# Kernel tuning notes

Measured on AMD Instinct MI355X. Metric: run time of the kernel, lower is better.

## Reference

```python
import jax, jax.numpy as jnp
import numpy as np

NUM_EMBEDDINGS = 512
EMBEDDING_DIM = 64
COMMITMENT_COST = 0.25


def setup_inputs() -> dict:
    key = jax.random.key(0)
    k1, k2, k3 = jax.random.split(key, 3)
    inputs = jax.random.normal(k1, (32, 64, 64, 64), dtype=jnp.float32)  # NCHW, C=embedding_dim
    labels = jax.random.randint(k2, (32,), 0, 12, dtype=jnp.int64 if jax.config.jax_enable_x64 else jnp.int32)
    # embedding initialized uniform(-1/K, 1/K) as in the torch module
    embedding = jax.random.uniform(k3, (NUM_EMBEDDINGS, EMBEDDING_DIM), dtype=jnp.float32,
                                   minval=-1.0 / NUM_EMBEDDINGS, maxval=1.0 / NUM_EMBEDDINGS)
    return {"inputs": inputs, "labels": labels, "embedding": embedding}


def reference(inputs, labels, embedding):
    # inputs: [B, C, H, W] with C == EMBEDDING_DIM; labels unused (matches original forward)
    x = jnp.transpose(inputs, (0, 2, 3, 1))            # [B, H, W, C]
    input_shape = x.shape
    flat = x.reshape(-1, EMBEDDING_DIM)                # [N, D]

    distances = (jnp.sum(flat * flat, axis=1, keepdims=True)
                 + jnp.sum(embedding * embedding, axis=1)
                 - 2.0 * jnp.matmul(flat, embedding.T))
    encoding_indices = jnp.argmin(distances, axis=1)   # [N]
    encodings = jax.nn.one_hot(encoding_indices, NUM_EMBEDDINGS, dtype=inputs.dtype)  # [N, K]

    # gather is the same math as encodings @ embedding, without the dense matmul
    quantized = embedding[encoding_indices].reshape(input_shape)  # [B, H, W, C]

    e_latent_loss = jnp.mean((jax.lax.stop_gradient(quantized) - x) ** 2)
    q_latent_loss = jnp.mean((quantized - jax.lax.stop_gradient(x)) ** 2)
    loss = q_latent_loss + COMMITMENT_COST * e_latent_loss

    # straight-through estimator
    quantized_st = x + jax.lax.stop_gradient(quantized - x)

    avg_probs = jnp.mean(encodings, axis=0)
    perplexity = jnp.exp(-jnp.sum(avg_probs * jnp.log(avg_probs + 1e-10)))

    return (loss, jnp.transpose(quantized_st, (0, 3, 1, 2)), perplexity, encodings)
```

## Files before the change

### kernel.cpp

```cpp
#include <hip/hip_runtime.h>


#define OFF_Q    1
#define OFF_PERP 8388609
#define OFF_ENC  8388610

typedef float accf4 __attribute__((ext_vector_type(4)));
typedef short bfrag8 __attribute__((ext_vector_type(8)));

__device__ __forceinline__ unsigned short f2bf(float f) {
    union { float f; unsigned u; } v; v.f = f;
    unsigned r = v.u + 0x7FFFu + ((v.u >> 16) & 1u);
    return (unsigned short)(r >> 16);
}

__device__ __forceinline__ void lds_barrier() {
    asm volatile("s_waitcnt lgkmcnt(0)" ::: "memory");
    __builtin_amdgcn_s_barrier();
    asm volatile("" ::: "memory");
}

__global__ __launch_bounds__(512) void vq_prep(const float* __restrict__ emb,
                                               float* __restrict__ Bk,
                                               unsigned* __restrict__ counts) {
    int k = threadIdx.x;
    const float4* e4 = reinterpret_cast<const float4*>(emb) + k * 16;
    float s = 0.f;
    #pragma unroll
    for (int i = 0; i < 16; ++i) {
        float4 v = e4[i];
        s += v.x * v.x + v.y * v.y + v.z * v.z + v.w * v.w;
    }
    Bk[k] = s;
    counts[k] = 0u;
}

__global__ __launch_bounds__(512, 4) void vq_dist(const float* __restrict__ in,
                                                  const float* __restrict__ emb,
                                                  const float* __restrict__ Bk,
                                                  int* __restrict__ idx,
                                                  float* __restrict__ lossPart,
                                                  float* __restrict__ out) {
    __shared__ __align__(16) unsigned short xB[64 * 72];
    __shared__ float sdw[8][64];
    __shared__ int   skw[8][64];
    __shared__ float lossW[8];

    const int tid  = (int)threadIdx.x;
    const int lane = tid & 63;
    const int v    = __builtin_amdgcn_readfirstlane(tid >> 6);
    const int q    = lane >> 4;
    const int cidx = lane & 15;

    bfrag8 efr[4][2];
    #pragma unroll
    for (int tn = 0; tn < 4; ++tn) {
        #pragma unroll
        for (int ks = 0; ks < 2; ++ks) {
            const float* ep = emb + (size_t)(v * 64 + tn * 16 + cidx) * 64 + ks * 32 + q * 8;
            float4 e0 = *reinterpret_cast<const float4*>(ep);
            float4 e1 = *reinterpret_cast<const float4*>(ep + 4);
            bfrag8 b;
            b[0] = (short)f2bf(e0.x); b[1] = (short)f2bf(e0.y);
            b[2] = (short)f2bf(e0.z); b[3] = (short)f2bf(e0.w);
            b[4] = (short)f2bf(e1.x); b[5] = (short)f2bf(e1.y);
            b[6] = (short)f2bf(e1.z); b[7] = (short)f2bf(e1.w);
            efr[tn][ks] = b;
        }
    }
    float4 Bn[4];
    #pragma unroll
    for (int tn = 0; tn < 4; ++tn)
        Bn[tn] = *reinterpret_cast<const float4*>(&Bk[v * 64 + tn * 16 + q * 4]);
    const int kbaseLane = v * 64 + q * 4;

    float lacc = 0.f;

    #pragma unroll 1
    for (int g = 0; g < 4; ++g) {
        const int gab = (int)blockIdx.x * 4 + g;
        const int bb  = gab >> 6;
        const int hh  = gab & 63;
        const size_t rowBase = (size_t)bb * 262144 + (size_t)hh * 64 + (size_t)lane;

        bfrag8 xpk;
        #pragma unroll
        for (int cc = 0; cc < 8; ++cc) {
            const float val = in[rowBase + (size_t)(v * 8 + cc) * 4096];
            lacc += val * val;
            xpk[cc] = (short)f2bf(val);
        }
        *reinterpret_cast<bfrag8*>(&xB[lane * 72 + v * 8]) = xpk;
        lds_barrier();

        #pragma unroll
        for (int rt = 0; rt < 4; ++rt) {
            const bfrag8 x0 = *reinterpret_cast<const bfrag8*>(&xB[(rt * 16 + cidx) * 72 + q * 8]);
            const bfrag8 x1 = *reinterpret_cast<const bfrag8*>(&xB[(rt * 16 + cidx) * 72 + 32 + q * 8]);
            accf4 acc[4];
            #pragma unroll
            for (int tn = 0; tn < 4; ++tn) {
                acc[tn] = (accf4){0.f, 0.f, 0.f, 0.f};
                acc[tn] = __builtin_amdgcn_mfma_f32_16x16x32_bf16(efr[tn][0], x0, acc[tn], 0, 0, 0);
                acc[tn] = __builtin_amdgcn_mfma_f32_16x16x32_bf16(efr[tn][1], x1, acc[tn], 0, 0, 0);
            }
            float best = 3.4e38f; int bk = kbaseLane;
            #pragma unroll
            for (int tn = 0; tn < 4; ++tn) {
                #pragma unroll
                for (int r = 0; r < 4; ++r) {
                    const float Bj = (r == 0) ? Bn[tn].x : (r == 1) ? Bn[tn].y : (r == 2) ? Bn[tn].z : Bn[tn].w;
                    const float d = Bj - 2.0f * acc[tn][r];
                    if (d < best) { best = d; bk = kbaseLane + tn * 16 + r; }
                }
            }
            #pragma unroll
            for (int s = 16; s <= 32; s <<= 1) {
                const float od = __shfl_xor(best, s);
                const int   ok = __shfl_xor(bk, s);
                if (od < best || (od == best && ok < bk)) { best = od; bk = ok; }
            }
            if (q == 0) {
                sdw[v][rt * 16 + cidx] = best;
                skw[v][rt * 16 + cidx] = bk;
            }
        }
        lds_barrier();

        if (v == 0) {
            float fd = sdw[0][lane];
            int   fk = skw[0][lane];
            #pragma unroll
            for (int vv = 1; vv < 8; ++vv) {
                const float dv = sdw[vv][lane];
                const int   kv = skw[vv][lane];
                if (dv < fd) { fd = dv; fk = kv; }
            }
            idx[gab * 64 + lane] = fk;
            lacc += fd;
        }
    }

    #pragma unroll
    for (int off = 32; off > 0; off >>= 1) lacc += __shfl_down(lacc, off);
    if (lane == 0) lossW[v] = lacc;
    lds_barrier();
    if (tid == 0) {
        float s = 0.f;
        #pragma unroll
        for (int i = 0; i < 8; ++i) s += lossW[i];
        lossPart[blockIdx.x] = s;
    }
}

__global__ __launch_bounds__(256) void vq_enc(const int* __restrict__ idx,
                                              const float* __restrict__ emb,
                                              unsigned* __restrict__ counts,
                                              float* __restrict__ out) {
    __shared__ int ki[64];
    __shared__ float eqL[64 * 68];

    const int tid = (int)threadIdx.x;
    const int gab = (int)blockIdx.x;
    const int bb  = gab >> 6;
    const int hh  = gab & 63;

    if (tid < 64) ki[tid] = idx[gab * 64 + tid];
    __syncthreads();
    if (tid < 64) atomicAdd(&counts[ki[tid]], 1u);

    {
        const int row = tid >> 2, seg = tid & 3;
        const float4* ep = reinterpret_cast<const float4*>(emb + (size_t)ki[row] * 64 + seg * 16);
        float4* dst = reinterpret_cast<float4*>(&eqL[row * 68 + seg * 16]);
        #pragma unroll
        for (int i = 0; i < 4; ++i) dst[i] = ep[i];
    }
    __syncthreads();

    {
        const int w = tid & 63, cq = tid >> 6;
        const size_t qBase = OFF_Q + (size_t)bb * 262144 + (size_t)hh * 64 + (size_t)w;
        #pragma unroll
        for (int cc = 0; cc < 16; ++cc) {
            const int c = cq * 16 + cc;
            out[qBase + (size_t)c * 4096] = eqL[w * 68 + c];
        }
    }

    const int rh = tid >> 7;
    const int j2 = tid & 127;
    float2* enc2 = reinterpret_cast<float2*>(out + OFF_ENC + (size_t)gab * 32768);

    #pragma unroll 4
    for (int r2 = 0; r2 < 32; ++r2) {
        const int row = r2 * 2 + rh;
        const int k = ki[row];
        #pragma unroll
        for (int half = 0; half < 2; ++half) {
            const int jj = j2 + half * 128;
            float2 val;
            val.x = ((k >> 1) == jj && (k & 1) == 0) ? 1.0f : 0.0f;
            val.y = ((k >> 1) == jj && (k & 1) == 1) ? 1.0f : 0.0f;
            enc2[(size_t)row * 256 + jj] = val;
        }
    }
}

__global__ __launch_bounds__(512) void vq_fin(const unsigned* __restrict__ counts,
                                              const float* __restrict__ lossPart,
                                              float* __restrict__ out) {
    __shared__ float red[512];
    __shared__ float lr[512];
    int k = threadIdx.x;
    float p = (float)counts[k] * (1.0f / 131072.0f);
    red[k] = p * logf(p + 1e-10f);
    lr[k] = lossPart[k];
    __syncthreads();
    for (int s = 256; s > 0; s >>= 1) {
        if (k < s) { red[k] += red[k + s]; lr[k] += lr[k + s]; }
        __syncthreads();
    }
    if (k == 0) {
        out[OFF_PERP] = expf(-red[0]);
        float mf = lr[0] * (1.0f / 8388608.0f);
        out[0] = mf + 0.25f * mf;
    }
}

extern "C" void kernel_launch(void* const* d_in, const int* in_sizes, int n_in,
                              void* d_out, int out_size, void* d_ws, size_t ws_size,
                              hipStream_t stream) {
    const float* in  = (const float*)d_in[0];
    const float* emb = (const float*)d_in[2];
    float* out = (float*)d_out;

    float* Bk        = (float*)d_ws;
    unsigned* counts = (unsigned*)((char*)d_ws + 2048);
    float* lossPart  = (float*)((char*)d_ws + 4096);
    int* idx         = (int*)((char*)d_ws + 8192);

    vq_prep<<<1, 512, 0, stream>>>(emb, Bk, counts);
    vq_dist<<<512, 512, 0, stream>>>(in, emb, Bk, idx, lossPart, out);
    vq_enc<<<2048, 256, 0, stream>>>(idx, emb, counts, out);
    vq_fin<<<1, 512, 0, stream>>>(counts, lossPart, out);
}
```

Measured before the change: 119.7 us.

## Restructure VQ distance kernel: per-wave row tiles, stream pre-converted bf16 codebook

The distance kernel switches from splitting the codebook across 8 waves with register-resident embedding fragments to having each wave own 32 input rows and loop over all 512 codes. The codebook is converted to bf16 once in the prep kernel and streamed from global/L2. This removes the LDS staging of inputs, two block barriers and the cross-wave argmin reduction per group. In exchange, each wave re-reads the whole bf16 codebook, and the grid doubles to 1024 blocks of 256 threads, so the loss partials are summed over 1024 entries.

```diff
diff --git a/kernel.cpp b/kernel.cpp
--- a/kernel.cpp
+++ b/kernel.cpp
@@ -22,133 +22,106 @@
 
 __global__ __launch_bounds__(512) void vq_prep(const float* __restrict__ emb,
                                                float* __restrict__ Bk,
-                                               unsigned* __restrict__ counts) {
+                                               unsigned* __restrict__ counts,
+                                               unsigned* __restrict__ embB) {
     int k = threadIdx.x;
     const float4* e4 = reinterpret_cast<const float4*>(emb) + k * 16;
+    uint2* dst = reinterpret_cast<uint2*>(embB) + k * 16;
     float s = 0.f;
     #pragma unroll
     for (int i = 0; i < 16; ++i) {
         float4 v = e4[i];
         s += v.x * v.x + v.y * v.y + v.z * v.z + v.w * v.w;
+        uint2 p;
+        p.x = (unsigned)f2bf(v.x) | ((unsigned)f2bf(v.y) << 16);
+        p.y = (unsigned)f2bf(v.z) | ((unsigned)f2bf(v.w) << 16);
+        dst[i] = p;
     }
     Bk[k] = s;
     counts[k] = 0u;
 }
 
-__global__ __launch_bounds__(512, 4) void vq_dist(const float* __restrict__ in,
-                                                  const float* __restrict__ emb,
+__global__ __launch_bounds__(256, 4) void vq_dist(const float* __restrict__ in,
+                                                  const unsigned short* __restrict__ embB,
                                                   const float* __restrict__ Bk,
                                                   int* __restrict__ idx,
-                                                  float* __restrict__ lossPart,
-                                                  float* __restrict__ out) {
-    __shared__ __align__(16) unsigned short xB[64 * 72];
-    __shared__ float sdw[8][64];
-    __shared__ int   skw[8][64];
-    __shared__ float lossW[8];
+                                                  float* __restrict__ lossPart) {
+    __shared__ float lossW[4];
 
     const int tid  = (int)threadIdx.x;
     const int lane = tid & 63;
-    const int v    = __builtin_amdgcn_readfirstlane(tid >> 6);
+    const int wv   = tid >> 6;
     const int q    = lane >> 4;
     const int cidx = lane & 15;
 
-    bfrag8 efr[4][2];
-    #pragma unroll
-    for (int tn = 0; tn < 4; ++tn) {
+    const int t  = (int)blockIdx.x * 4 + wv;
+    const int bb = t >> 7;
+    const int hh = (t >> 1) & 63;
+    const int wh = t & 1;
+    const size_t base = (size_t)bb * 262144 + (size_t)hh * 64 + (size_t)wh * 32;
+
+    float lacc = 0.f;
+    bfrag8 xf[2][2];
+    #pragma unroll
+    for (int rt = 0; rt < 2; ++rt) {
         #pragma unroll
         for (int ks = 0; ks < 2; ++ks) {
-            const float* ep = emb + (size_t)(v * 64 + tn * 16 + cidx) * 64 + ks * 32 + q * 8;
-            float4 e0 = *reinterpret_cast<const float4*>(ep);
-            float4 e1 = *reinterpret_cast<const float4*>(ep + 4);
-            bfrag8 b;
-            b[0] = (short)f2bf(e0.x); b[1] = (short)f2bf(e0.y);
-            b[2] = (short)f2bf(e0.z); b[3] = (short)f2bf(e0.w);
-            b[4] = (short)f2bf(e1.x); b[5] = (short)f2bf(e1.y);
-            b[6] = (short)f2bf(e1.z); b[7] = (short)f2bf(e1.w);
-            efr[tn][ks] = b;
-        }
-    }
-    float4 Bn[4];
-    #pragma unroll
-    for (int tn = 0; tn < 4; ++tn)
-        Bn[tn] = *reinterpret_cast<const float4*>(&Bk[v * 64 + tn * 16 + q * 4]);
-    const int kbaseLane = v * 64 + q * 4;
-
-    float lacc = 0.f;
-
-    #pragma unroll 1
-    for (int g = 0; g < 4; ++g) {
-        const int gab = (int)blockIdx.x * 4 + g;
-        const int bb  = gab >> 6;
-        const int hh  = gab & 63;
-        const size_t rowBase = (size_t)bb * 262144 + (size_t)hh * 64 + (size_t)lane;
-
-        bfrag8 xpk;
-        #pragma unroll
-        for (int cc = 0; cc < 8; ++cc) {
-            const float val = in[rowBase + (size_t)(v * 8 + cc) * 4096];
-            lacc += val * val;
-            xpk[cc] = (short)f2bf(val);
-        }
-        *reinterpret_cast<bfrag8*>(&xB[lane * 72 + v * 8]) = xpk;
-        lds_barrier();
-
-        #pragma unroll
-        for (int rt = 0; rt < 4; ++rt) {
-            const bfrag8 x0 = *reinterpret_cast<const bfrag8*>(&xB[(rt * 16 + cidx) * 72 + q * 8]);
-            const bfrag8 x1 = *reinterpret_cast<const bfrag8*>(&xB[(rt * 16 + cidx) * 72 + 32 + q * 8]);
-            accf4 acc[4];
             #pragma unroll
-            for (int tn = 0; tn < 4; ++tn) {
-                acc[tn] = (accf4){0.f, 0.f, 0.f, 0.f};
-                acc[tn] = __builtin_amdgcn_mfma_f32_16x16x32_bf16(efr[tn][0], x0, acc[tn], 0, 0, 0);
-                acc[tn] = __builtin_amdgcn_mfma_f32_16x16x32_bf16(efr[tn][1], x1, acc[tn], 0, 0, 0);
+            for (int i = 0; i < 8; ++i) {
+                const float val = in[base + (size_t)(ks * 32 + q * 8 + i) * 4096 + rt * 16 + cidx];
+                lacc += val * val;
+                xf[rt][ks][i] = (short)f2bf(val);
             }
-            float best = 3.4e38f; int bk = kbaseLane;
-            #pragma unroll
-            for (int tn = 0; tn < 4; ++tn) {
-                #pragma unroll
-                for (int r = 0; r < 4; ++r) {
-                    const float Bj = (r == 0) ? Bn[tn].x : (r == 1) ? Bn[tn].y : (r == 2) ? Bn[tn].z : Bn[tn].w;
-                    const float d = Bj - 2.0f * acc[tn][r];
-                    if (d < best) { best = d; bk = kbaseLane + tn * 16 + r; }
-                }
-            }
-            #pragma unroll
-            for (int s = 16; s <= 32; s <<= 1) {
-                const float od = __shfl_xor(best, s);
-                const int   ok = __shfl_xor(bk, s);
-                if (od < best || (od == best && ok < bk)) { best = od; bk = ok; }
-            }
-            if (q == 0) {
-                sdw[v][rt * 16 + cidx] = best;
-                skw[v][rt * 16 + cidx] = bk;
-            }
-        }
-        lds_barrier();
-
-        if (v == 0) {
-            float fd = sdw[0][lane];
-            int   fk = skw[0][lane];
-            #pragma unroll
-            for (int vv = 1; vv < 8; ++vv) {
-                const float dv = sdw[vv][lane];
-                const int   kv = skw[vv][lane];
-                if (dv < fd) { fd = dv; fk = kv; }
-            }
-            idx[gab * 64 + lane] = fk;
-            lacc += fd;
-        }
+        }
+    }
+
+    float best0 = 3.4e38f, best1 = 3.4e38f;
+    int   bk0 = q * 4,     bk1 = q * 4;
+
+    #pragma unroll 4
+    for (int tile = 0; tile < 32; ++tile) {
+        const bfrag8 e0 = *reinterpret_cast<const bfrag8*>(&embB[(tile * 16 + cidx) * 64 + q * 8]);
+        const bfrag8 e1 = *reinterpret_cast<const bfrag8*>(&embB[(tile * 16 + cidx) * 64 + 32 + q * 8]);
+        accf4 a0 = (accf4){0.f, 0.f, 0.f, 0.f};
+        accf4 a1 = (accf4){0.f, 0.f, 0.f, 0.f};
+        a0 = __builtin_amdgcn_mfma_f32_16x16x32_bf16(e0, xf[0][0], a0, 0, 0, 0);
+        a0 = __builtin_amdgcn_mfma_f32_16x16x32_bf16(e1, xf[0][1], a0, 0, 0, 0);
+        a1 = __builtin_amdgcn_mfma_f32_16x16x32_bf16(e0, xf[1][0], a1, 0, 0, 0);
+        a1 = __builtin_amdgcn_mfma_f32_16x16x32_bf16(e1, xf[1][1], a1, 0, 0, 0);
+
+        const float4 B4 = *reinterpret_cast<const float4*>(&Bk[tile * 16 + q * 4]);
+        #pragma unroll
+        for (int r = 0; r < 4; ++r) {
+            const float Bj = (r == 0) ? B4.x : (r == 1) ? B4.y : (r == 2) ? B4.z : B4.w;
+            const int k = tile * 16 + q * 4 + r;
+            const float d0 = Bj - 2.0f * a0[r];
+            if (d0 < best0) { best0 = d0; bk0 = k; }
+            const float d1 = Bj - 2.0f * a1[r];
+            if (d1 < best1) { best1 = d1; bk1 = k; }
+        }
+    }
+
+    #pragma unroll
+    for (int s = 16; s <= 32; s <<= 1) {
+        float od = __shfl_xor(best0, s); int ok = __shfl_xor(bk0, s);
+        if (od < best0 || (od == best0 && ok < bk0)) { best0 = od; bk0 = ok; }
+        od = __shfl_xor(best1, s); ok = __shfl_xor(bk1, s);
+        if (od < best1 || (od == best1 && ok < bk1)) { best1 = od; bk1 = ok; }
+    }
+    if (q == 0) {
+        idx[t * 32 + cidx]      = bk0;
+        idx[t * 32 + 16 + cidx] = bk1;
+        lacc += best0 + best1;
     }
 
     #pragma unroll
     for (int off = 32; off > 0; off >>= 1) lacc += __shfl_down(lacc, off);
-    if (lane == 0) lossW[v] = lacc;
+    if (lane == 0) lossW[wv] = lacc;
     lds_barrier();
     if (tid == 0) {
         float s = 0.f;
         #pragma unroll
-        for (int i = 0; i < 8; ++i) s += lossW[i];
+        for (int i = 0; i < 4; ++i) s += lossW[i];
         lossPart[blockIdx.x] = s;
     }
 }
@@ -215,7 +188,7 @@
     int k = threadIdx.x;
     float p = (float)counts[k] * (1.0f / 131072.0f);
     red[k] = p * logf(p + 1e-10f);
-    lr[k] = lossPart[k];
+    lr[k] = lossPart[k] + lossPart[k + 512];
     __syncthreads();
     for (int s = 256; s > 0; s >>= 1) {
         if (k < s) { red[k] += red[k + s]; lr[k] += lr[k + s]; }
@@ -235,13 +208,14 @@
     const float* emb = (const float*)d_in[2];
     float* out = (float*)d_out;
 
-    float* Bk        = (float*)d_ws;
-    unsigned* counts = (unsigned*)((char*)d_ws + 2048);
-    float* lossPart  = (float*)((char*)d_ws + 4096);
-    int* idx         = (int*)((char*)d_ws + 8192);
-
-    vq_prep<<<1, 512, 0, stream>>>(emb, Bk, counts);
-    vq_dist<<<512, 512, 0, stream>>>(in, emb, Bk, idx, lossPart, out);
+    float* Bk                 = (float*)d_ws;
+    unsigned* counts          = (unsigned*)((char*)d_ws + 2048);
+    float* lossPart           = (float*)((char*)d_ws + 4096);
+    unsigned* embB            = (unsigned*)((char*)d_ws + 8192);
+    int* idx                  = (int*)((char*)d_ws + 73728);
+
+    vq_prep<<<1, 512, 0, stream>>>(emb, Bk, counts, embB);
+    vq_dist<<<1024, 256, 0, stream>>>(in, (const unsigned short*)embB, Bk, idx, lossPart);
     vq_enc<<<2048, 256, 0, stream>>>(idx, emb, counts, out);
     vq_fin<<<1, 512, 0, stream>>>(counts, lossPart, out);
 }
```

Result: slower. 141.8 us (+18.5%).
